# Performance work log

Hardware: AMD Instinct MI355X
Metric: run time of the kernel (lower is better)

The kernel has to match this reference:

```python
import jax, jax.numpy as jnp
import numpy as np

N_SEG = 2048
SEG_LEN = 512
D = 128


def setup_inputs() -> dict:
    key = jax.random.key(0)
    k1, = jax.random.split(key, 1)
    total = N_SEG * SEG_LEN
    x = jax.random.normal(k1, (total, D), dtype=jnp.float32)
    # sizes must sum to total_tokens; use uniform segment lengths
    sizes = jnp.full((N_SEG,), SEG_LEN, dtype=jnp.int64)
    return {"x": x, "sizes": sizes, "window_size": 3}


def reference(x, sizes, window_size):
    # Segment-prefix max: for segment i (rows [start_i, start_i+sizes_i)),
    # reduce max over the first sizes_i - window_size + 1 rows.
    n = sizes.shape[0]
    total = x.shape[0]
    ends = jnp.cumsum(sizes)            # [n] exclusive end of each segment
    starts = ends - sizes               # [n] start offset of each segment
    pos = jnp.arange(total)             # [total]
    seg_id = jnp.searchsorted(ends, pos, side="right")  # [total] segment of each row
    pos_in_seg = pos - starts[seg_id]
    valid = pos_in_seg < (sizes[seg_id] - window_size + 1)
    # route invalid (tail-of-window) rows to a dummy segment that is dropped
    ids = jnp.where(valid, seg_id, n)
    out = jax.ops.segment_max(x, ids, num_segments=n + 1)  # [n+1, D]
    return out[:n]
```

## Files before the change

kernel.cpp:

```cpp
#include <hip/hip_runtime.h>
#include <hip/hip_bf16.h>
#include <math.h>


#define BLOCK 256

__device__ __forceinline__ float4 fmax4(float4 a, float4 b) {
    return make_float4(fmaxf(a.x, b.x), fmaxf(a.y, b.y),
                       fmaxf(a.z, b.z), fmaxf(a.w, b.w));
}

__global__ __launch_bounds__(BLOCK)
void seg_prefix_max_kernel(const float* __restrict__ x,
                           const int* __restrict__ sizes,
                           const int* __restrict__ wptr,
                           float* __restrict__ out,
                           int n_seg, int D) {
    const int seg = blockIdx.x;
    const int tid = threadIdx.x;
    const int w   = *wptr;

    __shared__ int red[BLOCK];
    int partial = 0;
    for (int j = tid; j < seg; j += BLOCK) partial += sizes[j];
    red[tid] = partial;
    __syncthreads();
    for (int s = BLOCK / 2; s > 0; s >>= 1) {
        if (tid < s) red[tid] += red[tid + s];
        __syncthreads();
    }
    const int start = red[0];
    const int L     = sizes[seg] - w + 1;

    const int nc4  = D >> 2;
    const int col4 = tid & 31;
    const int rg   = tid >> 5;

    float4 acc = make_float4(-INFINITY, -INFINITY, -INFINITY, -INFINITY);

    if (col4 < nc4) {
        const float4* xrow = (const float4*)x + (size_t)start * nc4 + col4;
        #pragma unroll 4
        for (int r = rg; r < L; r += 8) {
            float4 v = xrow[(size_t)r * nc4];
            acc = fmax4(acc, v);
        }
    }

    __shared__ float4 part[8][32];
    if (col4 < nc4) part[rg][col4] = acc;
    __syncthreads();

    if (tid < nc4) {
        float4 a = part[0][tid];
        #pragma unroll
        for (int j = 1; j < 8; ++j) a = fmax4(a, part[j][tid]);
        ((float4*)out)[(size_t)seg * nc4 + tid] = a;
    }
}

extern "C" void kernel_launch(void* const* d_in, const int* in_sizes, int n_in,
                              void* d_out, int out_size, void* d_ws, size_t ws_size,
                              hipStream_t stream) {
    const float* x     = (const float*)d_in[0];
    const int*   sizes = (const int*)d_in[1];
    const int*   wptr  = (const int*)d_in[2];
    float*       out   = (float*)d_out;

    const int n_seg = in_sizes[1];
    const int D     = out_size / n_seg;

    seg_prefix_max_kernel<<<n_seg, BLOCK, 0, stream>>>(x, sizes, wptr, out, n_seg, D);
}
```

Measured before the change: 672.7 us.

## Precompute segment starts with a scan kernel and split segments across two blocks

Replaces the per-block O(n_seg) prefix sum over sizes with a single-block exclusive scan kernel that writes segment starts to workspace. Each segment is then split into two row slices handled by separate blocks that write partial maxima, and a third kernel combines them. The aim is to remove redundant quadratic prefix work and add more blocks for memory parallelism, at the cost of two extra kernel launches and a partials buffer round-trip. The loop unroll is also raised from 4 to 8.

```diff
diff --git a/kernel.cpp b/kernel.cpp
--- a/kernel.cpp
+++ b/kernel.cpp
@@ -3,7 +3,8 @@
 #include <math.h>
 
 
-#define BLOCK 256
+#define BLOCK  256
+#define SLICES 2
 
 __device__ __forceinline__ float4 fmax4(float4 a, float4 b) {
     return make_float4(fmaxf(a.x, b.x), fmaxf(a.y, b.y),
@@ -11,40 +12,58 @@
 }
 
 __global__ __launch_bounds__(BLOCK)
-void seg_prefix_max_kernel(const float* __restrict__ x,
-                           const int* __restrict__ sizes,
-                           const int* __restrict__ wptr,
-                           float* __restrict__ out,
-                           int n_seg, int D) {
-    const int seg = blockIdx.x;
+void scan_kernel(const int* __restrict__ sizes, int* __restrict__ starts,
+                 int n_seg) {
+    __shared__ int sums[BLOCK];
     const int tid = threadIdx.x;
-    const int w   = *wptr;
-
-    __shared__ int red[BLOCK];
-    int partial = 0;
-    for (int j = tid; j < seg; j += BLOCK) partial += sizes[j];
-    red[tid] = partial;
+    const int per = (n_seg + BLOCK - 1) / BLOCK;
+    const int lo  = tid * per;
+    const int hi  = min(lo + per, n_seg);
+    int s = 0;
+    for (int i = lo; i < hi; ++i) s += sizes[i];
+    sums[tid] = s;
     __syncthreads();
-    for (int s = BLOCK / 2; s > 0; s >>= 1) {
-        if (tid < s) red[tid] += red[tid + s];
+    for (int off = 1; off < BLOCK; off <<= 1) {
+        int v = (tid >= off) ? sums[tid - off] : 0;
+        __syncthreads();
+        if (tid >= off) sums[tid] += v;
         __syncthreads();
     }
-    const int start = red[0];
-    const int L     = sizes[seg] - w + 1;
+    int base = (tid == 0) ? 0 : sums[tid - 1];
+    for (int i = lo; i < hi; ++i) {
+        starts[i] = base;
+        base += sizes[i];
+    }
+}
 
-    const int nc4  = D >> 2;
+__global__ __launch_bounds__(BLOCK)
+void seg_max_kernel(const float* __restrict__ x,
+                    const int* __restrict__ sizes,
+                    const int* __restrict__ starts,
+                    const int* __restrict__ wptr,
+                    float* __restrict__ partials,
+                    int nc4) {
+    const int b     = blockIdx.x;
+    const int seg   = b / SLICES;
+    const int slice = b % SLICES;
+    const int tid   = threadIdx.x;
+
+    const int L     = sizes[seg] - *wptr + 1;
+    const long long start = starts[seg];
+    const int lo = (int)(((long long)slice * L) / SLICES);
+    const int hi = (int)(((long long)(slice + 1) * L) / SLICES);
+    const int n  = hi - lo;
+
     const int col4 = tid & 31;
     const int rg   = tid >> 5;
 
     float4 acc = make_float4(-INFINITY, -INFINITY, -INFINITY, -INFINITY);
 
     if (col4 < nc4) {
-        const float4* xrow = (const float4*)x + (size_t)start * nc4 + col4;
-        #pragma unroll 4
-        for (int r = rg; r < L; r += 8) {
-            float4 v = xrow[(size_t)r * nc4];
-            acc = fmax4(acc, v);
-        }
+        const float4* xb = (const float4*)x + (size_t)(start + lo) * nc4 + col4;
+        #pragma unroll 8
+        for (int r = rg; r < n; r += 8)
+            acc = fmax4(acc, xb[(size_t)r * nc4]);
     }
 
     __shared__ float4 part[8][32];
@@ -55,8 +74,23 @@
         float4 a = part[0][tid];
         #pragma unroll
         for (int j = 1; j < 8; ++j) a = fmax4(a, part[j][tid]);
-        ((float4*)out)[(size_t)seg * nc4 + tid] = a;
+        ((float4*)partials)[((size_t)seg * SLICES + slice) * nc4 + tid] = a;
     }
+}
+
+__global__ __launch_bounds__(BLOCK)
+void combine_kernel(const float* __restrict__ partials,
+                    float* __restrict__ out,
+                    int total4, int nc4) {
+    const int i = blockIdx.x * BLOCK + threadIdx.x;
+    if (i >= total4) return;
+    const int seg = i / nc4;
+    const int c   = i - seg * nc4;
+    const float4* p = (const float4*)partials + (size_t)seg * SLICES * nc4 + c;
+    float4 a = p[0];
+    #pragma unroll
+    for (int j = 1; j < SLICES; ++j) a = fmax4(a, p[(size_t)j * nc4]);
+    ((float4*)out)[i] = a;
 }
 
 extern "C" void kernel_launch(void* const* d_in, const int* in_sizes, int n_in,
@@ -69,6 +103,15 @@
 
     const int n_seg = in_sizes[1];
     const int D     = out_size / n_seg;
+    const int nc4   = D >> 2;
 
-    seg_prefix_max_kernel<<<n_seg, BLOCK, 0, stream>>>(x, sizes, wptr, out, n_seg, D);
+    int*   starts   = (int*)d_ws;
+    float* partials = (float*)((char*)d_ws + 16384);
+
+    scan_kernel<<<1, BLOCK, 0, stream>>>(sizes, starts, n_seg);
+    seg_max_kernel<<<n_seg * SLICES, BLOCK, 0, stream>>>(x, sizes, starts, wptr,
+                                                         partials, nc4);
+    const int total4 = n_seg * nc4;
+    combine_kernel<<<(total4 + BLOCK - 1) / BLOCK, BLOCK, 0, stream>>>(
+        partials, out, total4, nc4);
 }
```

Result: no change. 680.6 us (+1.2%).
